# Optimization experiments

Hardware: AMD Instinct MI355X
Metric: run time of the kernel (lower is better)

The kernel has to match this reference:

```python
import jax, jax.numpy as jnp
import numpy as np

N_NODES = 100000
N_EDGES = 640000
NODE_D = 128   # node_emb_dim == edge_type_emb_dim (required by reverse-net input dim)
MSG_D = 128


def setup_inputs() -> dict:
    key = jax.random.key(0)
    ks = jax.random.split(key, 10)
    cat_d = 3 * NODE_D  # 2*node_emb + edge_type_emb
    s_msg = 1.0 / np.sqrt(cat_d)
    s_upd = 1.0 / np.sqrt(MSG_D)
    return {
        "node_features": jax.random.normal(ks[0], (N_NODES, NODE_D), jnp.float32),
        "edge_features": jax.random.normal(ks[1], (N_EDGES, NODE_D), jnp.float32),
        "from_idx": jax.random.randint(ks[2], (N_EDGES,), 0, N_NODES, jnp.int32),
        "to_idx": jax.random.randint(ks[3], (N_EDGES,), 0, N_NODES, jnp.int32),
        # message net (Linear + ReLU)
        "W_msg": jax.random.uniform(ks[4], (cat_d, MSG_D), jnp.float32, -s_msg, s_msg),
        "b_msg": jnp.zeros((MSG_D,), jnp.float32),
        # reverse message net (separate params)
        "W_rev": jax.random.uniform(ks[5], (cat_d, MSG_D), jnp.float32, -s_msg, s_msg),
        "b_rev": jnp.zeros((MSG_D,), jnp.float32),
        # node-update MLP (Linear + ReLU), residual update
        "W_upd": jax.random.uniform(ks[6], (MSG_D, NODE_D), jnp.float32, -s_upd, s_upd),
        "b_upd": jnp.zeros((NODE_D,), jnp.float32),
    }


def reference(node_features, edge_features, from_idx, to_idx,
              W_msg, b_msg, W_rev, b_rev, W_upd, b_upd):
    # gather endpoints and concat with edge features: [n_edges, 3*node_d]
    edge_inputs = jnp.concatenate(
        [node_features[from_idx], node_features[to_idx], edge_features], axis=-1)
    # forward + reverse message nets (same inputs, different params), summed
    messages = (jax.nn.relu(edge_inputs @ W_msg + b_msg)
                + jax.nn.relu(edge_inputs @ W_rev + b_rev))
    # scatter-sum into destination nodes: [n_nodes, msg_d]
    aggregated = jax.ops.segment_sum(messages, to_idx, num_segments=N_NODES)
    # residual node update: node + MLP(agg)
    return node_features + jax.nn.relu(aggregated @ W_upd + b_upd)
```

## Files before the change

### kernel.cpp

```cpp
#include <hip/hip_runtime.h>
#include <hip/hip_bf16.h>

#define N_NODES 100000
#define N_EDGES 640000

typedef __bf16 bf16_t;
typedef __bf16 bf16x8 __attribute__((ext_vector_type(8)));
typedef float f32x4 __attribute__((ext_vector_type(4)));
typedef float f4 __attribute__((ext_vector_type(4)));
typedef unsigned int u32x4 __attribute__((ext_vector_type(4)));

__device__ __forceinline__ float bflo(unsigned int u) { return __uint_as_float(u << 16); }
__device__ __forceinline__ float bfhi(unsigned int u) { return __uint_as_float(u & 0xffff0000u); }
__device__ __forceinline__ unsigned int bfpack(float a, float b) {
    union { bf16_t h[2]; unsigned int u; } pk;
    pk.h[0] = (bf16_t)a; pk.h[1] = (bf16_t)b;
    return pk.u;
}

__global__ void hist_kernel(const int* __restrict__ to_idx, int* __restrict__ hist) {
    int e = blockIdx.x * 256 + threadIdx.x;
    if (e < N_EDGES) atomicAdd(&hist[to_idx[e]], 1);
}

#define SCAN_CH 1000

__global__ __launch_bounds__(1024)
void scan_reduce_kernel(const int* __restrict__ hist, int* __restrict__ bsum) {
    __shared__ int red[1024];
    int b = blockIdx.x, t = threadIdx.x;
    int v = (t < SCAN_CH) ? hist[b * SCAN_CH + t] : 0;
    red[t] = v;
    __syncthreads();
    for (int off = 512; off > 0; off >>= 1) {
        if (t < off) red[t] += red[t + off];
        __syncthreads();
    }
    if (t == 0) bsum[b] = red[0];
}

__global__ __launch_bounds__(128)
void scan_base_kernel(const int* __restrict__ bsum, int* __restrict__ bbase) {
    __shared__ int s[128];
    int t = threadIdx.x;
    int v = (t < 100) ? bsum[t] : 0;
    s[t] = v;
    __syncthreads();
    for (int off = 1; off < 128; off <<= 1) {
        int u = (t >= off) ? s[t - off] : 0;
        __syncthreads();
        s[t] += u;
        __syncthreads();
    }
    if (t < 100) bbase[t] = s[t] - v;
}

__global__ __launch_bounds__(1024)
void scan_final_kernel(const int* __restrict__ hist,
                       const int* __restrict__ bbase,
                       int* __restrict__ cursor,
                       int* __restrict__ row_start) {
    __shared__ int s[1024];
    int b = blockIdx.x, t = threadIdx.x;
    int v = (t < SCAN_CH) ? hist[b * SCAN_CH + t] : 0;
    s[t] = v;
    __syncthreads();
    for (int off = 1; off < 1024; off <<= 1) {
        int u = (t >= off) ? s[t - off] : 0;
        __syncthreads();
        s[t] += u;
        __syncthreads();
    }
    int excl = bbase[b] + s[t] - v;
    if (t < SCAN_CH) {
        cursor[b * SCAN_CH + t] = excl;
        row_start[b * SCAN_CH + t] = excl;
    }
    if (b == 99 && t == SCAN_CH - 1) row_start[N_NODES] = excl + v;
}

__global__ void inv_scatter_kernel(const int* __restrict__ to_idx,
                                   int* __restrict__ cursor,
                                   int* __restrict__ inv) {
    int e = blockIdx.x * 256 + threadIdx.x;
    if (e < N_EDGES) {
        int pos = atomicAdd(&cursor[to_idx[e]], 1);
        inv[e] = pos;
    }
}

__global__ void prep_w_new(const float* __restrict__ Wmsg,
                           const float* __restrict__ Wrev,
                           const float* __restrict__ Wupd,
                           bf16_t* __restrict__ Wt1,
                           bf16_t* __restrict__ WtE,
                           bf16_t* __restrict__ WtU) {
    int idx = blockIdx.x * 256 + threadIdx.x;
    if (idx < 512 * 128) {
        int p = idx >> 7, k = idx & 127;
        int blk = p >> 7, c = p & 127;
        float v;
        if (blk == 0)      v = Wmsg[k * 128 + c];
        else if (blk == 1) v = Wrev[k * 128 + c];
        else if (blk == 2) v = Wmsg[(128 + k) * 128 + c];
        else               v = Wrev[(128 + k) * 128 + c];
        Wt1[idx] = (bf16_t)v;
    }
    if (idx < 256 * 128) {
        int p = idx >> 7, k = idx & 127;
        float v = (p < 128) ? Wmsg[(256 + k) * 128 + p]
                            : Wrev[(256 + k) * 128 + (p - 128)];
        WtE[idx] = (bf16_t)v;
    }
    if (idx < 128 * 128) {
        int n = idx >> 7, p = idx & 127;
        int colp = 32 * (p >> 5) + ((p >> 1) & 15) + 16 * (p & 1);
        WtU[idx] = (bf16_t)Wupd[colp * 128 + n];
    }
}

__global__ __launch_bounds__(512, 4)
void proj_node_kernel(const float* __restrict__ nodef,
                      const bf16_t* __restrict__ Wt1,
                      unsigned int* __restrict__ A_u) {
    __shared__ char lds_raw[64 * 256];
    const int tid = threadIdx.x;
    const int nb = blockIdx.x * 64;
    const int by = blockIdx.y;

#pragma unroll
    for (int j = 0; j < 4; ++j) {
        int linear = tid + 512 * j;
        int r = linear >> 5, q = linear & 31;
        int node = nb + r;
        f4 v = (f4){0.f, 0.f, 0.f, 0.f};
        if (node < N_NODES)
            v = *reinterpret_cast<const f4*>(nodef + (size_t)node * 128 + q * 4);
        union { bf16_t b[4]; uint2 u; } pk;
        pk.b[0] = (bf16_t)v[0]; pk.b[1] = (bf16_t)v[1];
        pk.b[2] = (bf16_t)v[2]; pk.b[3] = (bf16_t)v[3];
        int byte = (r * 256 + q * 8) ^ ((r & 7) << 4);
        *reinterpret_cast<uint2*>(lds_raw + byte) = pk.u;
    }
    __syncthreads();

    const int wv = tid >> 6;
    const int wr = wv >> 2, wc = wv & 3;
    const int lane = tid & 63;
    const int lhi = lane >> 4, llo = lane & 15;

    f32x4 acc[2][4];
#pragma unroll
    for (int m = 0; m < 2; ++m)
#pragma unroll
        for (int n = 0; n < 4; ++n)
            acc[m][n] = (f32x4){0.f, 0.f, 0.f, 0.f};

    const bf16_t* bptr[4];
#pragma unroll
    for (int n = 0; n < 4; ++n) {
        int colb = (n < 2) ? (wc * 32 + 16 * n) : (128 + wc * 32 + 16 * (n - 2));
        bptr[n] = Wt1 + (size_t)(by * 256 + colb + llo) * 128 + lhi * 8;
    }

#pragma unroll
    for (int k0 = 0; k0 < 4; ++k0) {
        bf16x8 a[2], b[4];
#pragma unroll
        for (int m = 0; m < 2; ++m) {
            int ra = wr * 32 + 16 * m + llo;
            int byte = (ra * 256 + (k0 * 32 + lhi * 8) * 2) ^ ((ra & 7) << 4);
            a[m] = *reinterpret_cast<const bf16x8*>(lds_raw + byte);
        }
#pragma unroll
        for (int n = 0; n < 4; ++n)
            b[n] = *reinterpret_cast<const bf16x8*>(bptr[n] + k0 * 32);
#pragma unroll
        for (int m = 0; m < 2; ++m)
#pragma unroll
            for (int n = 0; n < 4; ++n)
                acc[m][n] = __builtin_amdgcn_mfma_f32_16x16x32_bf16(a[m], b[n], acc[m][n], 0, 0, 0);
    }

    const int wli = wc * 16 + llo;
#pragma unroll
    for (int m = 0; m < 2; ++m) {
        int rbase = wr * 32 + 16 * m + lhi * 4;
#pragma unroll
        for (int r = 0; r < 4; ++r) {
            int node = nb + rbase + r;
            if (node < N_NODES) {
                size_t base = (size_t)node * 256 + by * 128;
                uint2 pr;
                pr.x = bfpack(acc[m][0][r], acc[m][1][r]);
                pr.y = bfpack(acc[m][2][r], acc[m][3][r]);
                *reinterpret_cast<uint2*>(A_u + base + 2 * wli) = pr;
            }
        }
    }
}

__global__ __launch_bounds__(256, 4)
void edge_fused_kernel(const float* __restrict__ edgef,
                       const int* __restrict__ from_idx,
                       const int* __restrict__ to_idx,
                       const int* __restrict__ inv,
                       const unsigned int* __restrict__ A_u,
                       const bf16_t* __restrict__ WtE,
                       const float* __restrict__ b_msg,
                       const float* __restrict__ b_rev,
                       unsigned int* __restrict__ msgs_u) {
    __shared__ char lds_raw[32 * 256];
    __shared__ int s_from[32], s_dst[32], s_inv[32];

    const int tid = threadIdx.x;
    const int eb = blockIdx.x * 32;

    if (tid < 32) {
        s_from[tid] = from_idx[eb + tid];
        s_dst[tid]  = to_idx[eb + tid];
        s_inv[tid]  = inv[eb + tid];
    }

#pragma unroll
    for (int j = 0; j < 4; ++j) {
        int linear = tid + 256 * j;
        int r = linear >> 5, q = linear & 31;
        f4 v = *reinterpret_cast<const f4*>(edgef + (size_t)(eb + r) * 128 + q * 4);
        union { bf16_t b[4]; uint2 u; } pk;
        pk.b[0] = (bf16_t)v[0]; pk.b[1] = (bf16_t)v[1];
        pk.b[2] = (bf16_t)v[2]; pk.b[3] = (bf16_t)v[3];
        int byte = (r * 256 + q * 8) ^ ((r & 7) << 4);
        *reinterpret_cast<uint2*>(lds_raw + byte) = pk.u;
    }
    __syncthreads();

    const int wc = tid >> 6;
    const int lane = tid & 63;
    const int lhi = lane >> 4, llo = lane & 15;
    const int wli = wc * 16 + llo;

    uint2 gF[2][4], gT[2][4];
#pragma unroll
    for (int m = 0; m < 2; ++m) {
#pragma unroll
        for (int r = 0; r < 4; ++r) {
            int rr = 16 * m + lhi * 4 + r;
            gF[m][r] = *reinterpret_cast<const uint2*>(
                A_u + (size_t)s_from[rr] * 256 + 2 * wli);
            gT[m][r] = *reinterpret_cast<const uint2*>(
                A_u + (size_t)s_dst[rr] * 256 + 128 + 2 * wli);
        }
    }

    f32x4 acc[2][4];
#pragma unroll
    for (int m = 0; m < 2; ++m)
#pragma unroll
        for (int n = 0; n < 4; ++n)
            acc[m][n] = (f32x4){0.f, 0.f, 0.f, 0.f};

    const bf16_t* bptr[4];
#pragma unroll
    for (int n = 0; n < 4; ++n) {
        int colb = (n < 2) ? (wc * 32 + 16 * n) : (128 + wc * 32 + 16 * (n - 2));
        bptr[n] = WtE + (size_t)(colb + llo) * 128 + lhi * 8;
    }

#pragma unroll
    for (int k0 = 0; k0 < 4; ++k0) {
        bf16x8 a[2], b[4];
#pragma unroll
        for (int m = 0; m < 2; ++m) {
            int ra = 16 * m + llo;
            int byte = (ra * 256 + (k0 * 32 + lhi * 8) * 2) ^ ((ra & 7) << 4);
            a[m] = *reinterpret_cast<const bf16x8*>(lds_raw + byte);
        }
#pragma unroll
        for (int n = 0; n < 4; ++n)
            b[n] = *reinterpret_cast<const bf16x8*>(bptr[n] + k0 * 32);
#pragma unroll
        for (int m = 0; m < 2; ++m)
#pragma unroll
            for (int n = 0; n < 4; ++n)
                acc[m][n] = __builtin_amdgcn_mfma_f32_16x16x32_bf16(a[m], b[n], acc[m][n], 0, 0, 0);
    }

    const int c0 = wc * 32 + llo;
    const float bm0 = b_msg[c0], bm1 = b_msg[c0 + 16];
    const float br0 = b_rev[c0], br1 = b_rev[c0 + 16];
#pragma unroll
    for (int m = 0; m < 2; ++m) {
#pragma unroll
        for (int r = 0; r < 4; ++r) {
            int rr = 16 * m + lhi * 4 + r;
            float m0 = fmaxf(acc[m][0][r] + bm0 + bflo(gF[m][r].x) + bflo(gT[m][r].x), 0.f);
            float m1 = fmaxf(acc[m][1][r] + bm1 + bfhi(gF[m][r].x) + bfhi(gT[m][r].x), 0.f);
            float r0 = fmaxf(acc[m][2][r] + br0 + bflo(gF[m][r].y) + bflo(gT[m][r].y), 0.f);
            float r1 = fmaxf(acc[m][3][r] + br1 + bfhi(gF[m][r].y) + bfhi(gT[m][r].y), 0.f);
            msgs_u[(size_t)s_inv[rr] * 64 + wli] = bfpack(m0 + r0, m1 + r1);
        }
    }
}

__global__ __launch_bounds__(256, 4)
void node_upd_kernel(const unsigned int* __restrict__ msgs_u,
                     const int* __restrict__ row_start,
                     const float* __restrict__ nodef,
                     const bf16_t* __restrict__ WtU,
                     const float* __restrict__ b_upd,
                     float* __restrict__ out) {
    __shared__ char lds_raw[64 * 256];
    __shared__ int s_rs[65];

    const int tid = threadIdx.x;
    const int nb = blockIdx.x * 64;

    if (tid < 65) {
        int nid = nb + tid;
        s_rs[tid] = (nid <= N_NODES) ? row_start[nid] : N_EDGES;
    }
    __syncthreads();

    {
        const int r = tid >> 2;
        const int q = tid & 3;
        float s[32];
#pragma unroll
        for (int i = 0; i < 32; ++i) s[i] = 0.f;
        const int rs = s_rs[r], re = s_rs[r + 1];
        int e = rs;
        for (; e + 1 < re; e += 2) {
            const u32x4* p0 = reinterpret_cast<const u32x4*>(msgs_u + (size_t)e * 64 + q * 16);
            const u32x4* p1 = reinterpret_cast<const u32x4*>(msgs_u + (size_t)(e + 1) * 64 + q * 16);
            u32x4 w0[4], w1[4];
#pragma unroll
            for (int i = 0; i < 4; ++i) { w0[i] = p0[i]; w1[i] = p1[i]; }
#pragma unroll
            for (int i = 0; i < 4; ++i) {
                s[8*i+0] += bflo(w0[i][0]) + bflo(w1[i][0]);
                s[8*i+1] += bfhi(w0[i][0]) + bfhi(w1[i][0]);
                s[8*i+2] += bflo(w0[i][1]) + bflo(w1[i][1]);
                s[8*i+3] += bfhi(w0[i][1]) + bfhi(w1[i][1]);
                s[8*i+4] += bflo(w0[i][2]) + bflo(w1[i][2]);
                s[8*i+5] += bfhi(w0[i][2]) + bfhi(w1[i][2]);
                s[8*i+6] += bflo(w0[i][3]) + bflo(w1[i][3]);
                s[8*i+7] += bfhi(w0[i][3]) + bfhi(w1[i][3]);
            }
        }
        if (e < re) {
            const u32x4* p = reinterpret_cast<const u32x4*>(msgs_u + (size_t)e * 64 + q * 16);
#pragma unroll
            for (int i = 0; i < 4; ++i) {
                u32x4 w = p[i];
                s[8*i+0] += bflo(w[0]); s[8*i+1] += bfhi(w[0]);
                s[8*i+2] += bflo(w[1]); s[8*i+3] += bfhi(w[1]);
                s[8*i+4] += bflo(w[2]); s[8*i+5] += bfhi(w[2]);
                s[8*i+6] += bflo(w[3]); s[8*i+7] += bfhi(w[3]);
            }
        }
#pragma unroll
        for (int i = 0; i < 4; ++i) {
            union { bf16_t b[8]; u32x4 u; } pk;
#pragma unroll
            for (int w = 0; w < 8; ++w) pk.b[w] = (bf16_t)s[8*i + w];
            int byte = (r * 256 + q * 64 + i * 16) ^ ((r & 7) << 4);
            *reinterpret_cast<u32x4*>(lds_raw + byte) = pk.u;
        }
    }
    __syncthreads();

    const int wv = tid >> 6;
    const int lane = tid & 63;
    const int lhi = lane >> 4, llo = lane & 15;

    f32x4 acc[4][2];
#pragma unroll
    for (int m = 0; m < 4; ++m)
#pragma unroll
        for (int n = 0; n < 2; ++n)
            acc[m][n] = (f32x4){0.f, 0.f, 0.f, 0.f};

#pragma unroll
    for (int k0 = 0; k0 < 4; ++k0) {
        bf16x8 a[4], b[2];
#pragma unroll
        for (int m = 0; m < 4; ++m) {
            int ra = 16 * m + llo;
            int byte = (ra * 256 + (k0 * 32 + lhi * 8) * 2) ^ ((ra & 7) << 4);
            a[m] = *reinterpret_cast<const bf16x8*>(lds_raw + byte);
        }
#pragma unroll
        for (int n = 0; n < 2; ++n) {
            int col = wv * 32 + 16 * n + llo;
            b[n] = *reinterpret_cast<const bf16x8*>(WtU + (size_t)col * 128 + k0 * 32 + lhi * 8);
        }
#pragma unroll
        for (int m = 0; m < 4; ++m)
#pragma unroll
            for (int n = 0; n < 2; ++n)
                acc[m][n] = __builtin_amdgcn_mfma_f32_16x16x32_bf16(a[m], b[n], acc[m][n], 0, 0, 0);
    }

#pragma unroll
    for (int m = 0; m < 4; ++m) {
        int rbase = 16 * m + lhi * 4;
#pragma unroll
        for (int r = 0; r < 4; ++r) {
            int i = nb + rbase + r;
            if (i < N_NODES) {
#pragma unroll
                for (int n = 0; n < 2; ++n) {
                    int c = wv * 32 + 16 * n + llo;
                    out[(size_t)i * 128 + c] =
                        nodef[(size_t)i * 128 + c]
                        + fmaxf(acc[m][n][r] + b_upd[c], 0.f);
                }
            }
        }
    }
}

__global__ __launch_bounds__(256)
void convert_nodef_kernel(const float* __restrict__ nodef,
                          unsigned short* __restrict__ nodef_bf) {
    int i = blockIdx.x * 256 + threadIdx.x;
    if (i < N_NODES * 32) {
        f4 v = *reinterpret_cast<const f4*>(nodef + (size_t)i * 4);
        union { bf16_t b[4]; unsigned long long ll; } pk;
        pk.b[0] = (bf16_t)v[0]; pk.b[1] = (bf16_t)v[1];
        pk.b[2] = (bf16_t)v[2]; pk.b[3] = (bf16_t)v[3];
        *reinterpret_cast<unsigned long long*>(nodef_bf + (size_t)i * 4) = pk.ll;
    }
}

__global__ void prep_w_old(const float* __restrict__ Wmsg,
                           const float* __restrict__ Wrev,
                           const float* __restrict__ Wupd,
                           bf16_t* __restrict__ WtAB,
                           bf16_t* __restrict__ WtU) {
    int idx = blockIdx.x * 256 + threadIdx.x;
    if (idx < 256 * 384) {
        int n = idx / 384;
        int k = idx - n * 384;
        float v = (n < 128) ? Wmsg[k * 128 + n] : Wrev[k * 128 + (n - 128)];
        WtAB[idx] = (bf16_t)v;
    }
    if (idx < 128 * 128) {
        int n = idx >> 7, p = idx & 127;
        int colp = 32 * (p >> 5) + ((p >> 1) & 15) + 16 * (p & 1);
        WtU[idx] = (bf16_t)Wupd[colp * 128 + n];
    }
}

__global__ __launch_bounds__(512, 4)
void edge_msg_old_kernel(const unsigned short* __restrict__ nodef_bf,
                         const float* __restrict__ edgef,
                         const int* __restrict__ from_idx,
                         const int* __restrict__ to_idx,
                         const int* __restrict__ inv,
                         const bf16_t* __restrict__ WtAB,
                         const float* __restrict__ b_msg,
                         const float* __restrict__ b_rev,
                         unsigned int* __restrict__ msgs_u) {
    __shared__ char lds_raw[64 * 384];
    __shared__ int s_from[64], s_dst[64], s_inv[64];

    const int tid = threadIdx.x;
    const int eb = blockIdx.x * 64;

    if (tid < 64) {
        s_from[tid] = from_idx[eb + tid];
        s_dst[tid]  = to_idx[eb + tid];
        s_inv[tid]  = inv[eb + tid];
    }

    const int wv = tid >> 6;
    const int wr = wv >> 2, wc = wv & 3;
    const int lane = tid & 63;
    const int lhi = lane >> 4, llo = lane & 15;

    f32x4 acc[2][4];
#pragma unroll
    for (int m = 0; m < 2; ++m)
#pragma unroll
        for (int n = 0; n < 4; ++n)
            acc[m][n] = (f32x4){0.f, 0.f, 0.f, 0.f};

    const bf16_t* bptr[4];
#pragma unroll
    for (int n = 0; n < 4; ++n) {
        int colb = (n < 2) ? (wc * 32 + 16 * n) : (128 + wc * 32 + 16 * (n - 2));
        bptr[n] = WtAB + (size_t)(colb + llo) * 384 + lhi * 8;
    }

    __syncthreads();

#pragma unroll
    for (int j = 0; j < 3; ++j) {
        int linear = tid + 512 * j;
        int r = linear / 24;
        int q = linear - r * 24;
        const u32x4* src = (q < 16)
            ? reinterpret_cast<const u32x4*>(nodef_bf + (size_t)s_from[r] * 128) + q
            : reinterpret_cast<const u32x4*>(nodef_bf + (size_t)s_dst[r] * 128) + (q - 16);
        u32x4 v = *src;
        int byte = (r * 384 + q * 16) ^ ((r & 7) << 4);
        *reinterpret_cast<u32x4*>(lds_raw + byte) = v;
    }
    __syncthreads();

#pragma unroll
    for (int k0 = 0; k0 < 6; ++k0) {
        bf16x8 a[2], b[4];
#pragma unroll
        for (int m = 0; m < 2; ++m) {
            int ra = wr * 32 + 16 * m + llo;
            int byte = (ra * 384 + k0 * 64 + lhi * 16) ^ ((ra & 7) << 4);
            a[m] = *reinterpret_cast<const bf16x8*>(lds_raw + byte);
        }
#pragma unroll
        for (int n = 0; n < 4; ++n)
            b[n] = *reinterpret_cast<const bf16x8*>(bptr[n] + k0 * 32);
#pragma unroll
        for (int m = 0; m < 2; ++m)
#pragma unroll
            for (int n = 0; n < 4; ++n)
                acc[m][n] = __builtin_amdgcn_mfma_f32_16x16x32_bf16(a[m], b[n], acc[m][n], 0, 0, 0);
    }
    __syncthreads();

#pragma unroll
    for (int j = 0; j < 3; ++j) {
        int linear = tid + 512 * j;
        int r = linear / 24;
        int qq = linear - r * 24;
        u32x4 w;
        if (qq < 8) {
            w = *(reinterpret_cast<const u32x4*>(nodef_bf + (size_t)s_dst[r] * 128) + 8 + qq);
        } else {
            int c = qq - 8;
            const f4* ep = reinterpret_cast<const f4*>(edgef + (size_t)(eb + r) * 128 + c * 8);
            f4 v0 = ep[0];
            f4 v1 = ep[1];
            union { bf16_t b[8]; u32x4 u; } pk;
            pk.b[0] = (bf16_t)v0[0]; pk.b[1] = (bf16_t)v0[1];
            pk.b[2] = (bf16_t)v0[2]; pk.b[3] = (bf16_t)v0[3];
            pk.b[4] = (bf16_t)v1[0]; pk.b[5] = (bf16_t)v1[1];
            pk.b[6] = (bf16_t)v1[2]; pk.b[7] = (bf16_t)v1[3];
            w = pk.u;
        }
        int byte = (r * 384 + qq * 16) ^ ((r & 7) << 4);
        *reinterpret_cast<u32x4*>(lds_raw + byte) = w;
    }
    __syncthreads();

#pragma unroll
    for (int k0 = 0; k0 < 6; ++k0) {
        bf16x8 a[2], b[4];
#pragma unroll
        for (int m = 0; m < 2; ++m) {
            int ra = wr * 32 + 16 * m + llo;
            int byte = (ra * 384 + k0 * 64 + lhi * 16) ^ ((ra & 7) << 4);
            a[m] = *reinterpret_cast<const bf16x8*>(lds_raw + byte);
        }
#pragma unroll
        for (int n = 0; n < 4; ++n)
            b[n] = *reinterpret_cast<const bf16x8*>(bptr[n] + (6 + k0) * 32);
#pragma unroll
        for (int m = 0; m < 2; ++m)
#pragma unroll
            for (int n = 0; n < 4; ++n)
                acc[m][n] = __builtin_amdgcn_mfma_f32_16x16x32_bf16(a[m], b[n], acc[m][n], 0, 0, 0);
    }

    const int c0 = wc * 32 + llo;
    const float bm0 = b_msg[c0], br0 = b_rev[c0];
    const float bm1 = b_msg[c0 + 16], br1 = b_rev[c0 + 16];
#pragma unroll
    for (int m = 0; m < 2; ++m) {
        int rbase = wr * 32 + 16 * m + lhi * 4;
#pragma unroll
        for (int r = 0; r < 4; ++r) {
            float v0 = fmaxf(acc[m][0][r] + bm0, 0.f) + fmaxf(acc[m][2][r] + br0, 0.f);
            float v1 = fmaxf(acc[m][1][r] + bm1, 0.f) + fmaxf(acc[m][3][r] + br1, 0.f);
            msgs_u[(size_t)s_inv[rbase + r] * 64 + wc * 16 + llo] = bfpack(v0, v1);
        }
    }
}

extern "C" void kernel_launch(void* const* d_in, const int* in_sizes, int n_in,
                              void* d_out, int out_size, void* d_ws, size_t ws_size,
                              hipStream_t stream) {
    const float* nodef    = (const float*)d_in[0];
    const float* edgef    = (const float*)d_in[1];
    const int*   from_idx = (const int*)d_in[2];
    const int*   to_idx   = (const int*)d_in[3];
    const float* Wmsg     = (const float*)d_in[4];
    const float* bmsg     = (const float*)d_in[5];
    const float* Wrev     = (const float*)d_in[6];
    const float* brev     = (const float*)d_in[7];
    const float* Wupd     = (const float*)d_in[8];
    const float* bupd     = (const float*)d_in[9];
    float* out = (float*)d_out;
    char* ws = (char*)d_ws;

    if (ws_size >= 271000000) {
        unsigned int* A_u      = (unsigned int*)ws;
        unsigned int* msgs_u   = (unsigned int*)(ws + 102400000);
        bf16_t*       Wt1      = (bf16_t*)(ws + 266240000);
        bf16_t*       WtE      = (bf16_t*)(ws + 266371072);
        bf16_t*       WtU      = (bf16_t*)(ws + 266436608);
        int*          hist     = (int*)(ws + 266469376);
        int*          cursor   = (int*)(ws + 266869376);
        int*          rowstart = (int*)(ws + 267269376);
        int*          inv      = (int*)(ws + 267669392);
        int*          bsum     = (int*)(ws + 270229392);
        int*          bbase    = (int*)(ws + 270229792);

        hipMemsetAsync(hist, 0, (size_t)N_NODES * sizeof(int), stream);
        prep_w_new<<<256, 256, 0, stream>>>(Wmsg, Wrev, Wupd, Wt1, WtE, WtU);
        hist_kernel<<<(N_EDGES + 255) / 256, 256, 0, stream>>>(to_idx, hist);
        scan_reduce_kernel<<<100, 1024, 0, stream>>>(hist, bsum);
        scan_base_kernel<<<1, 128, 0, stream>>>(bsum, bbase);
        scan_final_kernel<<<100, 1024, 0, stream>>>(hist, bbase, cursor, rowstart);
        inv_scatter_kernel<<<(N_EDGES + 255) / 256, 256, 0, stream>>>(to_idx, cursor, inv);
        proj_node_kernel<<<dim3((N_NODES + 63) / 64, 2), 512, 0, stream>>>(nodef, Wt1, A_u);
        edge_fused_kernel<<<N_EDGES / 32, 256, 0, stream>>>(
            edgef, from_idx, to_idx, inv, A_u, WtE, bmsg, brev, msgs_u);
        node_upd_kernel<<<(N_NODES + 63) / 64, 256, 0, stream>>>(
            msgs_u, rowstart, nodef, WtU, bupd, out);
    } else {
        unsigned int*   msgs_u   = (unsigned int*)ws;
        bf16_t*         WtAB     = (bf16_t*)(ws + 163840000);
        bf16_t*         WtU      = (bf16_t*)(ws + 164036608);
        unsigned short* nodef_bf = (unsigned short*)(ws + 164069376);
        int*            hist     = (int*)(ws + 189669376);
        int*            cursor   = (int*)(ws + 190069376);
        int*            rowstart = (int*)(ws + 190469376);
        int*            inv      = (int*)(ws + 190869392);
        int*            bsum     = (int*)(ws + 193429392);
        int*            bbase    = (int*)(ws + 193429792);

        hipMemsetAsync(hist, 0, (size_t)N_NODES * sizeof(int), stream);
        convert_nodef_kernel<<<12500, 256, 0, stream>>>(nodef, nodef_bf);
        prep_w_old<<<384, 256, 0, stream>>>(Wmsg, Wrev, Wupd, WtAB, WtU);
        hist_kernel<<<(N_EDGES + 255) / 256, 256, 0, stream>>>(to_idx, hist);
        scan_reduce_kernel<<<100, 1024, 0, stream>>>(hist, bsum);
        scan_base_kernel<<<1, 128, 0, stream>>>(bsum, bbase);
        scan_final_kernel<<<100, 1024, 0, stream>>>(hist, bbase, cursor, rowstart);
        inv_scatter_kernel<<<(N_EDGES + 255) / 256, 256, 0, stream>>>(to_idx, cursor, inv);
        edge_msg_old_kernel<<<N_EDGES / 64, 512, 0, stream>>>(
            nodef_bf, edgef, from_idx, to_idx, inv, WtAB, bmsg, brev, msgs_u);
        node_upd_kernel<<<(N_NODES + 63) / 64, 256, 0, stream>>>(
            msgs_u, rowstart, nodef, WtU, bupd, out);
    }
}
```

Before: 457.8 us.

## Defer to-node projection add and ReLU into node update kernel

The edge kernel no longer gathers the destination-node projection. It stores pre-activation forward and reverse message sums (two bf16 channels each) in CSR order. The node update kernel loads the destination projection once per node and adds it to every incoming edge before the two ReLUs and the aggregation. This removes a random gather per edge, but doubles the size of the intermediate message buffer and needs a larger workspace, otherwise it falls back to the old path.

```diff
diff --git a/kernel.cpp b/kernel.cpp
--- a/kernel.cpp
+++ b/kernel.cpp
@@ -201,24 +201,22 @@
 }
 
 __global__ __launch_bounds__(256, 4)
-void edge_fused_kernel(const float* __restrict__ edgef,
-                       const int* __restrict__ from_idx,
-                       const int* __restrict__ to_idx,
-                       const int* __restrict__ inv,
-                       const unsigned int* __restrict__ A_u,
-                       const bf16_t* __restrict__ WtE,
-                       const float* __restrict__ b_msg,
-                       const float* __restrict__ b_rev,
-                       unsigned int* __restrict__ msgs_u) {
+void edge_fused_defT(const float* __restrict__ edgef,
+                     const int* __restrict__ from_idx,
+                     const int* __restrict__ inv,
+                     const unsigned int* __restrict__ A_u,
+                     const bf16_t* __restrict__ WtE,
+                     const float* __restrict__ b_msg,
+                     const float* __restrict__ b_rev,
+                     unsigned int* __restrict__ msgs2) {
     __shared__ char lds_raw[32 * 256];
-    __shared__ int s_from[32], s_dst[32], s_inv[32];
+    __shared__ int s_from[32], s_inv[32];
 
     const int tid = threadIdx.x;
     const int eb = blockIdx.x * 32;
 
     if (tid < 32) {
         s_from[tid] = from_idx[eb + tid];
-        s_dst[tid]  = to_idx[eb + tid];
         s_inv[tid]  = inv[eb + tid];
     }
 
@@ -240,9 +238,232 @@
     const int lhi = lane >> 4, llo = lane & 15;
     const int wli = wc * 16 + llo;
 
+    uint2 gF[2][4];
+#pragma unroll
+    for (int m = 0; m < 2; ++m)
+#pragma unroll
+        for (int r = 0; r < 4; ++r) {
+            int rr = 16 * m + lhi * 4 + r;
+            gF[m][r] = *reinterpret_cast<const uint2*>(
+                A_u + (size_t)s_from[rr] * 256 + 2 * wli);
+        }
+
+    f32x4 acc[2][4];
+#pragma unroll
+    for (int m = 0; m < 2; ++m)
+#pragma unroll
+        for (int n = 0; n < 4; ++n)
+            acc[m][n] = (f32x4){0.f, 0.f, 0.f, 0.f};
+
+    const bf16_t* bptr[4];
+#pragma unroll
+    for (int n = 0; n < 4; ++n) {
+        int colb = (n < 2) ? (wc * 32 + 16 * n) : (128 + wc * 32 + 16 * (n - 2));
+        bptr[n] = WtE + (size_t)(colb + llo) * 128 + lhi * 8;
+    }
+
+#pragma unroll
+    for (int k0 = 0; k0 < 4; ++k0) {
+        bf16x8 a[2], b[4];
+#pragma unroll
+        for (int m = 0; m < 2; ++m) {
+            int ra = 16 * m + llo;
+            int byte = (ra * 256 + (k0 * 32 + lhi * 8) * 2) ^ ((ra & 7) << 4);
+            a[m] = *reinterpret_cast<const bf16x8*>(lds_raw + byte);
+        }
+#pragma unroll
+        for (int n = 0; n < 4; ++n)
+            b[n] = *reinterpret_cast<const bf16x8*>(bptr[n] + k0 * 32);
+#pragma unroll
+        for (int m = 0; m < 2; ++m)
+#pragma unroll
+            for (int n = 0; n < 4; ++n)
+                acc[m][n] = __builtin_amdgcn_mfma_f32_16x16x32_bf16(a[m], b[n], acc[m][n], 0, 0, 0);
+    }
+
+    const int c0 = wc * 32 + llo;
+    const float bm0 = b_msg[c0], bm1 = b_msg[c0 + 16];
+    const float br0 = b_rev[c0], br1 = b_rev[c0 + 16];
+#pragma unroll
+    for (int m = 0; m < 2; ++m) {
+#pragma unroll
+        for (int r = 0; r < 4; ++r) {
+            int rr = 16 * m + lhi * 4 + r;
+            uint2 pw;
+            pw.x = bfpack(acc[m][0][r] + bm0 + bflo(gF[m][r].x),
+                          acc[m][1][r] + bm1 + bfhi(gF[m][r].x));
+            pw.y = bfpack(acc[m][2][r] + br0 + bflo(gF[m][r].y),
+                          acc[m][3][r] + br1 + bfhi(gF[m][r].y));
+            *reinterpret_cast<uint2*>(msgs2 + (size_t)s_inv[rr] * 128 + 2 * wli) = pw;
+        }
+    }
+}
+
+__global__ __launch_bounds__(256, 4)
+void node_upd_defT(const unsigned int* __restrict__ msgs2,
+                   const int* __restrict__ row_start,
+                   const unsigned int* __restrict__ A_u,
+                   const float* __restrict__ nodef,
+                   const bf16_t* __restrict__ WtU,
+                   const float* __restrict__ b_upd,
+                   float* __restrict__ out) {
+    __shared__ char lds_raw[64 * 256];
+    __shared__ int s_rs[65];
+
+    const int tid = threadIdx.x;
+    const int nb = blockIdx.x * 64;
+
+    if (tid < 65) {
+        int nid = nb + tid;
+        s_rs[tid] = (nid <= N_NODES) ? row_start[nid] : N_EDGES;
+    }
+    __syncthreads();
+
+    {
+        const int r = tid >> 2;
+        const int q = tid & 3;
+        u32x4 tw[8];
+        int node = nb + r;
+        if (node < N_NODES) {
+            const u32x4* tp = reinterpret_cast<const u32x4*>(
+                A_u + (size_t)node * 256 + 128 + q * 32);
+#pragma unroll
+            for (int j = 0; j < 8; ++j) tw[j] = tp[j];
+        } else {
+#pragma unroll
+            for (int j = 0; j < 8; ++j) tw[j] = (u32x4){0, 0, 0, 0};
+        }
+
+        float s[32];
+#pragma unroll
+        for (int i = 0; i < 32; ++i) s[i] = 0.f;
+        const int rs = s_rs[r], re = s_rs[r + 1];
+        for (int e = rs; e < re; ++e) {
+            const u32x4* p = reinterpret_cast<const u32x4*>(
+                msgs2 + (size_t)e * 128 + q * 32);
+#pragma unroll
+            for (int j = 0; j < 8; ++j) {
+                u32x4 v = p[j];
+                float m0 = fmaxf(bflo(v[0]) + bflo(tw[j][0]), 0.f);
+                float m1 = fmaxf(bfhi(v[0]) + bfhi(tw[j][0]), 0.f);
+                float r0 = fmaxf(bflo(v[1]) + bflo(tw[j][1]), 0.f);
+                float r1 = fmaxf(bfhi(v[1]) + bfhi(tw[j][1]), 0.f);
+                float n0 = fmaxf(bflo(v[2]) + bflo(tw[j][2]), 0.f);
+                float n1 = fmaxf(bfhi(v[2]) + bfhi(tw[j][2]), 0.f);
+                float o0 = fmaxf(bflo(v[3]) + bflo(tw[j][3]), 0.f);
+                float o1 = fmaxf(bfhi(v[3]) + bfhi(tw[j][3]), 0.f);
+                int sbase = 8 * (j >> 1) + 4 * (j & 1);
+                s[sbase + 0] += m0 + r0;
+                s[sbase + 1] += m1 + r1;
+                s[sbase + 2] += n0 + o0;
+                s[sbase + 3] += n1 + o1;
+            }
+        }
+#pragma unroll
+        for (int i = 0; i < 4; ++i) {
+            union { bf16_t b[8]; u32x4 u; } pk;
+#pragma unroll
+            for (int w = 0; w < 8; ++w) pk.b[w] = (bf16_t)s[8*i + w];
+            int byte = (r * 256 + q * 64 + i * 16) ^ ((r & 7) << 4);
+            *reinterpret_cast<u32x4*>(lds_raw + byte) = pk.u;
+        }
+    }
+    __syncthreads();
+
+    const int wv = tid >> 6;
+    const int lane = tid & 63;
+    const int lhi = lane >> 4, llo = lane & 15;
+
+    f32x4 acc[4][2];
+#pragma unroll
+    for (int m = 0; m < 4; ++m)
+#pragma unroll
+        for (int n = 0; n < 2; ++n)
+            acc[m][n] = (f32x4){0.f, 0.f, 0.f, 0.f};
+
+#pragma unroll
+    for (int k0 = 0; k0 < 4; ++k0) {
+        bf16x8 a[4], b[2];
+#pragma unroll
+        for (int m = 0; m < 4; ++m) {
+            int ra = 16 * m + llo;
+            int byte = (ra * 256 + (k0 * 32 + lhi * 8) * 2) ^ ((ra & 7) << 4);
+            a[m] = *reinterpret_cast<const bf16x8*>(lds_raw + byte);
+        }
+#pragma unroll
+        for (int n = 0; n < 2; ++n) {
+            int col = wv * 32 + 16 * n + llo;
+            b[n] = *reinterpret_cast<const bf16x8*>(WtU + (size_t)col * 128 + k0 * 32 + lhi * 8);
+        }
+#pragma unroll
+        for (int m = 0; m < 4; ++m)
+#pragma unroll
+            for (int n = 0; n < 2; ++n)
+                acc[m][n] = __builtin_amdgcn_mfma_f32_16x16x32_bf16(a[m], b[n], acc[m][n], 0, 0, 0);
+    }
+
+#pragma unroll
+    for (int m = 0; m < 4; ++m) {
+        int rbase = 16 * m + lhi * 4;
+#pragma unroll
+        for (int r = 0; r < 4; ++r) {
+            int i = nb + rbase + r;
+            if (i < N_NODES) {
+#pragma unroll
+                for (int n = 0; n < 2; ++n) {
+                    int c = wv * 32 + 16 * n + llo;
+                    out[(size_t)i * 128 + c] =
+                        nodef[(size_t)i * 128 + c]
+                        + fmaxf(acc[m][n][r] + b_upd[c], 0.f);
+                }
+            }
+        }
+    }
+}
+
+__global__ __launch_bounds__(256, 4)
+void edge_fused_full(const float* __restrict__ edgef,
+                     const int* __restrict__ from_idx,
+                     const int* __restrict__ to_idx,
+                     const int* __restrict__ inv,
+                     const unsigned int* __restrict__ A_u,
+                     const bf16_t* __restrict__ WtE,
+                     const float* __restrict__ b_msg,
+                     const float* __restrict__ b_rev,
+                     unsigned int* __restrict__ msgs_u) {
+    __shared__ char lds_raw[32 * 256];
+    __shared__ int s_from[32], s_dst[32], s_inv[32];
+
+    const int tid = threadIdx.x;
+    const int eb = blockIdx.x * 32;
+
+    if (tid < 32) {
+        s_from[tid] = from_idx[eb + tid];
+        s_dst[tid]  = to_idx[eb + tid];
+        s_inv[tid]  = inv[eb + tid];
+    }
+
+#pragma unroll
+    for (int j = 0; j < 4; ++j) {
+        int linear = tid + 256 * j;
+        int r = linear >> 5, q = linear & 31;
+        f4 v = *reinterpret_cast<const f4*>(edgef + (size_t)(eb + r) * 128 + q * 4);
+        union { bf16_t b[4]; uint2 u; } pk;
+        pk.b[0] = (bf16_t)v[0]; pk.b[1] = (bf16_t)v[1];
+        pk.b[2] = (bf16_t)v[2]; pk.b[3] = (bf16_t)v[3];
+        int byte = (r * 256 + q * 8) ^ ((r & 7) << 4);
+        *reinterpret_cast<uint2*>(lds_raw + byte) = pk.u;
+    }
+    __syncthreads();
+
+    const int wc = tid >> 6;
+    const int lane = tid & 63;
+    const int lhi = lane >> 4, llo = lane & 15;
+    const int wli = wc * 16 + llo;
+
     uint2 gF[2][4], gT[2][4];
 #pragma unroll
-    for (int m = 0; m < 2; ++m) {
+    for (int m = 0; m < 2; ++m)
 #pragma unroll
         for (int r = 0; r < 4; ++r) {
             int rr = 16 * m + lhi * 4 + r;
@@ -251,7 +472,6 @@
             gT[m][r] = *reinterpret_cast<const uint2*>(
                 A_u + (size_t)s_dst[rr] * 256 + 128 + 2 * wli);
         }
-    }
 
     f32x4 acc[2][4];
 #pragma unroll
@@ -304,12 +524,12 @@
 }
 
 __global__ __launch_bounds__(256, 4)
-void node_upd_kernel(const unsigned int* __restrict__ msgs_u,
-                     const int* __restrict__ row_start,
-                     const float* __restrict__ nodef,
-                     const bf16_t* __restrict__ WtU,
-                     const float* __restrict__ b_upd,
-                     float* __restrict__ out) {
+void node_upd_pk(const unsigned int* __restrict__ msgs_u,
+                 const int* __restrict__ row_start,
+                 const float* __restrict__ nodef,
+                 const bf16_t* __restrict__ WtU,
+                 const float* __restrict__ b_upd,
+                 float* __restrict__ out) {
     __shared__ char lds_raw[64 * 256];
     __shared__ int s_rs[65];
 
@@ -329,26 +549,7 @@
 #pragma unroll
         for (int i = 0; i < 32; ++i) s[i] = 0.f;
         const int rs = s_rs[r], re = s_rs[r + 1];
-        int e = rs;
-        for (; e + 1 < re; e += 2) {
-            const u32x4* p0 = reinterpret_cast<const u32x4*>(msgs_u + (size_t)e * 64 + q * 16);
-            const u32x4* p1 = reinterpret_cast<const u32x4*>(msgs_u + (size_t)(e + 1) * 64 + q * 16);
-            u32x4 w0[4], w1[4];
-#pragma unroll
-            for (int i = 0; i < 4; ++i) { w0[i] = p0[i]; w1[i] = p1[i]; }
-#pragma unroll
-            for (int i = 0; i < 4; ++i) {
-                s[8*i+0] += bflo(w0[i][0]) + bflo(w1[i][0]);
-                s[8*i+1] += bfhi(w0[i][0]) + bfhi(w1[i][0]);
-                s[8*i+2] += bflo(w0[i][1]) + bflo(w1[i][1]);
-                s[8*i+3] += bfhi(w0[i][1]) + bfhi(w1[i][1]);
-                s[8*i+4] += bflo(w0[i][2]) + bflo(w1[i][2]);
-                s[8*i+5] += bfhi(w0[i][2]) + bfhi(w1[i][2]);
-                s[8*i+6] += bflo(w0[i][3]) + bflo(w1[i][3]);
-                s[8*i+7] += bfhi(w0[i][3]) + bfhi(w1[i][3]);
-            }
-        }
-        if (e < re) {
+        for (int e = rs; e < re; ++e) {
             const u32x4* p = reinterpret_cast<const u32x4*>(msgs_u + (size_t)e * 64 + q * 16);
 #pragma unroll
             for (int i = 0; i < 4; ++i) {
@@ -417,174 +618,6 @@
                         + fmaxf(acc[m][n][r] + b_upd[c], 0.f);
                 }
             }
-        }
-    }
-}
-
-__global__ __launch_bounds__(256)
-void convert_nodef_kernel(const float* __restrict__ nodef,
-                          unsigned short* __restrict__ nodef_bf) {
-    int i = blockIdx.x * 256 + threadIdx.x;
-    if (i < N_NODES * 32) {
-        f4 v = *reinterpret_cast<const f4*>(nodef + (size_t)i * 4);
-        union { bf16_t b[4]; unsigned long long ll; } pk;
-        pk.b[0] = (bf16_t)v[0]; pk.b[1] = (bf16_t)v[1];
-        pk.b[2] = (bf16_t)v[2]; pk.b[3] = (bf16_t)v[3];
-        *reinterpret_cast<unsigned long long*>(nodef_bf + (size_t)i * 4) = pk.ll;
-    }
-}
-
-__global__ void prep_w_old(const float* __restrict__ Wmsg,
-                           const float* __restrict__ Wrev,
-                           const float* __restrict__ Wupd,
-                           bf16_t* __restrict__ WtAB,
-                           bf16_t* __restrict__ WtU) {
-    int idx = blockIdx.x * 256 + threadIdx.x;
-    if (idx < 256 * 384) {
-        int n = idx / 384;
-        int k = idx - n * 384;
-        float v = (n < 128) ? Wmsg[k * 128 + n] : Wrev[k * 128 + (n - 128)];
-        WtAB[idx] = (bf16_t)v;
-    }
-    if (idx < 128 * 128) {
-        int n = idx >> 7, p = idx & 127;
-        int colp = 32 * (p >> 5) + ((p >> 1) & 15) + 16 * (p & 1);
-        WtU[idx] = (bf16_t)Wupd[colp * 128 + n];
-    }
-}
-
-__global__ __launch_bounds__(512, 4)
-void edge_msg_old_kernel(const unsigned short* __restrict__ nodef_bf,
-                         const float* __restrict__ edgef,
-                         const int* __restrict__ from_idx,
-                         const int* __restrict__ to_idx,
-                         const int* __restrict__ inv,
-                         const bf16_t* __restrict__ WtAB,
-                         const float* __restrict__ b_msg,
-                         const float* __restrict__ b_rev,
-                         unsigned int* __restrict__ msgs_u) {
-    __shared__ char lds_raw[64 * 384];
-    __shared__ int s_from[64], s_dst[64], s_inv[64];
-
-    const int tid = threadIdx.x;
-    const int eb = blockIdx.x * 64;
-
-    if (tid < 64) {
-        s_from[tid] = from_idx[eb + tid];
-        s_dst[tid]  = to_idx[eb + tid];
-        s_inv[tid]  = inv[eb + tid];
-    }
-
-    const int wv = tid >> 6;
-    const int wr = wv >> 2, wc = wv & 3;
-    const int lane = tid & 63;
-    const int lhi = lane >> 4, llo = lane & 15;
-
-    f32x4 acc[2][4];
-#pragma unroll
-    for (int m = 0; m < 2; ++m)
-#pragma unroll
-        for (int n = 0; n < 4; ++n)
-            acc[m][n] = (f32x4){0.f, 0.f, 0.f, 0.f};
-
-    const bf16_t* bptr[4];
-#pragma unroll
-    for (int n = 0; n < 4; ++n) {
-        int colb = (n < 2) ? (wc * 32 + 16 * n) : (128 + wc * 32 + 16 * (n - 2));
-        bptr[n] = WtAB + (size_t)(colb + llo) * 384 + lhi * 8;
-    }
-
-    __syncthreads();
-
-#pragma unroll
-    for (int j = 0; j < 3; ++j) {
-        int linear = tid + 512 * j;
-        int r = linear / 24;
-        int q = linear - r * 24;
-        const u32x4* src = (q < 16)
-            ? reinterpret_cast<const u32x4*>(nodef_bf + (size_t)s_from[r] * 128) + q
-            : reinterpret_cast<const u32x4*>(nodef_bf + (size_t)s_dst[r] * 128) + (q - 16);
-        u32x4 v = *src;
-        int byte = (r * 384 + q * 16) ^ ((r & 7) << 4);
-        *reinterpret_cast<u32x4*>(lds_raw + byte) = v;
-    }
-    __syncthreads();
-
-#pragma unroll
-    for (int k0 = 0; k0 < 6; ++k0) {
-        bf16x8 a[2], b[4];
-#pragma unroll
-        for (int m = 0; m < 2; ++m) {
-            int ra = wr * 32 + 16 * m + llo;
-            int byte = (ra * 384 + k0 * 64 + lhi * 16) ^ ((ra & 7) << 4);
-            a[m] = *reinterpret_cast<const bf16x8*>(lds_raw + byte);
-        }
-#pragma unroll
-        for (int n = 0; n < 4; ++n)
-            b[n] = *reinterpret_cast<const bf16x8*>(bptr[n] + k0 * 32);
-#pragma unroll
-        for (int m = 0; m < 2; ++m)
-#pragma unroll
-            for (int n = 0; n < 4; ++n)
-                acc[m][n] = __builtin_amdgcn_mfma_f32_16x16x32_bf16(a[m], b[n], acc[m][n], 0, 0, 0);
-    }
-    __syncthreads();
-
-#pragma unroll
-    for (int j = 0; j < 3; ++j) {
-        int linear = tid + 512 * j;
-        int r = linear / 24;
-        int qq = linear - r * 24;
-        u32x4 w;
-        if (qq < 8) {
-            w = *(reinterpret_cast<const u32x4*>(nodef_bf + (size_t)s_dst[r] * 128) + 8 + qq);
-        } else {
-            int c = qq - 8;
-            const f4* ep = reinterpret_cast<const f4*>(edgef + (size_t)(eb + r) * 128 + c * 8);
-            f4 v0 = ep[0];
-            f4 v1 = ep[1];
-            union { bf16_t b[8]; u32x4 u; } pk;
-            pk.b[0] = (bf16_t)v0[0]; pk.b[1] = (bf16_t)v0[1];
-            pk.b[2] = (bf16_t)v0[2]; pk.b[3] = (bf16_t)v0[3];
-            pk.b[4] = (bf16_t)v1[0]; pk.b[5] = (bf16_t)v1[1];
-            pk.b[6] = (bf16_t)v1[2]; pk.b[7] = (bf16_t)v1[3];
-            w = pk.u;
-        }
-        int byte = (r * 384 + qq * 16) ^ ((r & 7) << 4);
-        *reinterpret_cast<u32x4*>(lds_raw + byte) = w;
-    }
-    __syncthreads();
-
-#pragma unroll
-    for (int k0 = 0; k0 < 6; ++k0) {
-        bf16x8 a[2], b[4];
-#pragma unroll
-        for (int m = 0; m < 2; ++m) {
-            int ra = wr * 32 + 16 * m + llo;
-            int byte = (ra * 384 + k0 * 64 + lhi * 16) ^ ((ra & 7) << 4);
-            a[m] = *reinterpret_cast<const bf16x8*>(lds_raw + byte);
-        }
-#pragma unroll
-        for (int n = 0; n < 4; ++n)
-            b[n] = *reinterpret_cast<const bf16x8*>(bptr[n] + (6 + k0) * 32);
-#pragma unroll
-        for (int m = 0; m < 2; ++m)
-#pragma unroll
-            for (int n = 0; n < 4; ++n)
-                acc[m][n] = __builtin_amdgcn_mfma_f32_16x16x32_bf16(a[m], b[n], acc[m][n], 0, 0, 0);
-    }
-
-    const int c0 = wc * 32 + llo;
-    const float bm0 = b_msg[c0], br0 = b_rev[c0];
-    const float bm1 = b_msg[c0 + 16], br1 = b_rev[c0 + 16];
-#pragma unroll
-    for (int m = 0; m < 2; ++m) {
-        int rbase = wr * 32 + 16 * m + lhi * 4;
-#pragma unroll
-        for (int r = 0; r < 4; ++r) {
-            float v0 = fmaxf(acc[m][0][r] + bm0, 0.f) + fmaxf(acc[m][2][r] + br0, 0.f);
-            float v1 = fmaxf(acc[m][1][r] + bm1, 0.f) + fmaxf(acc[m][3][r] + br1, 0.f);
-            msgs_u[(size_t)s_inv[rbase + r] * 64 + wc * 16 + llo] = bfpack(v0, v1);
         }
     }
 }
@@ -605,7 +638,32 @@
     float* out = (float*)d_out;
     char* ws = (char*)d_ws;
 
-    if (ws_size >= 271000000) {
+    if (ws_size >= 435000000) {
+        unsigned int* A_u      = (unsigned int*)ws;
+        unsigned int* msgs2    = (unsigned int*)(ws + 102400000);
+        bf16_t*       Wt1      = (bf16_t*)(ws + 430080000);
+        bf16_t*       WtE      = (bf16_t*)(ws + 430211072);
+        bf16_t*       WtU      = (bf16_t*)(ws + 430276608);
+        int*          hist     = (int*)(ws + 430309376);
+        int*          cursor   = (int*)(ws + 430709376);
+        int*          rowstart = (int*)(ws + 431109376);
+        int*          inv      = (int*)(ws + 431509392);
+        int*          bsum     = (int*)(ws + 434069392);
+        int*          bbase    = (int*)(ws + 434069792);
+
+        hipMemsetAsync(hist, 0, (size_t)N_NODES * sizeof(int), stream);
+        prep_w_new<<<256, 256, 0, stream>>>(Wmsg, Wrev, Wupd, Wt1, WtE, WtU);
+        hist_kernel<<<(N_EDGES + 255) / 256, 256, 0, stream>>>(to_idx, hist);
+        scan_reduce_kernel<<<100, 1024, 0, stream>>>(hist, bsum);
+        scan_base_kernel<<<1, 128, 0, stream>>>(bsum, bbase);
+        scan_final_kernel<<<100, 1024, 0, stream>>>(hist, bbase, cursor, rowstart);
+        inv_scatter_kernel<<<(N_EDGES + 255) / 256, 256, 0, stream>>>(to_idx, cursor, inv);
+        proj_node_kernel<<<dim3((N_NODES + 63) / 64, 2), 512, 0, stream>>>(nodef, Wt1, A_u);
+        edge_fused_defT<<<N_EDGES / 32, 256, 0, stream>>>(
+            edgef, from_idx, inv, A_u, WtE, bmsg, brev, msgs2);
+        node_upd_defT<<<(N_NODES + 63) / 64, 256, 0, stream>>>(
+            msgs2, rowstart, A_u, nodef, WtU, bupd, out);
+    } else {
         unsigned int* A_u      = (unsigned int*)ws;
         unsigned int* msgs_u   = (unsigned int*)(ws + 102400000);
         bf16_t*       Wt1      = (bf16_t*)(ws + 266240000);
@@ -626,33 +684,9 @@
         scan_final_kernel<<<100, 1024, 0, stream>>>(hist, bbase, cursor, rowstart);
         inv_scatter_kernel<<<(N_EDGES + 255) / 256, 256, 0, stream>>>(to_idx, cursor, inv);
         proj_node_kernel<<<dim3((N_NODES + 63) / 64, 2), 512, 0, stream>>>(nodef, Wt1, A_u);
-        edge_fused_kernel<<<N_EDGES / 32, 256, 0, stream>>>(
+        edge_fused_full<<<N_EDGES / 32, 256, 0, stream>>>(
             edgef, from_idx, to_idx, inv, A_u, WtE, bmsg, brev, msgs_u);
-        node_upd_kernel<<<(N_NODES + 63) / 64, 256, 0, stream>>>(
+        node_upd_pk<<<(N_NODES + 63) / 64, 256, 0, stream>>>(
             msgs_u, rowstart, nodef, WtU, bupd, out);
-    } else {
-        unsigned int*   msgs_u   = (unsigned int*)ws;
-        bf16_t*         WtAB     = (bf16_t*)(ws + 163840000);
-        bf16_t*         WtU      = (bf16_t*)(ws + 164036608);
-        unsigned short* nodef_bf = (unsigned short*)(ws + 164069376);
-        int*            hist     = (int*)(ws + 189669376);
-        int*            cursor   = (int*)(ws + 190069376);
-        int*            rowstart = (int*)(ws + 190469376);
-        int*            inv      = (int*)(ws + 190869392);
-        int*            bsum     = (int*)(ws + 193429392);
-        int*            bbase    = (int*)(ws + 193429792);
-
-        hipMemsetAsync(hist, 0, (size_t)N_NODES * sizeof(int), stream);
-        convert_nodef_kernel<<<12500, 256, 0, stream>>>(nodef, nodef_bf);
-        prep_w_old<<<384, 256, 0, stream>>>(Wmsg, Wrev, Wupd, WtAB, WtU);
-        hist_kernel<<<(N_EDGES + 255) / 256, 256, 0, stream>>>(to_idx, hist);
-        scan_reduce_kernel<<<100, 1024, 0, stream>>>(hist, bsum);
-        scan_base_kernel<<<1, 128, 0, stream>>>(bsum, bbase);
-        scan_final_kernel<<<100, 1024, 0, stream>>>(hist, bbase, cursor, rowstart);
-        inv_scatter_kernel<<<(N_EDGES + 255) / 256, 256, 0, stream>>>(to_idx, cursor, inv);
-        edge_msg_old_kernel<<<N_EDGES / 64, 512, 0, stream>>>(
-            nodef_bf, edgef, from_idx, to_idx, inv, WtAB, bmsg, brev, msgs_u);
-        node_upd_kernel<<<(N_NODES + 63) / 64, 256, 0, stream>>>(
-            msgs_u, rowstart, nodef, WtU, bupd, out);
-    }
-}
+    }
+}
```

Result: slower. 537.3 us (+17.4%).
